# Performance work log

Hardware: AMD Instinct MI355X
Metric: run time of the kernel (lower is better)

Reference implementation:

```python
import jax, jax.numpy as jnp
import numpy as np

N = 50257   # vocab size
D = 128     # embedding_dim
B = 2048    # batch
C = 10      # context window size


def setup_inputs() -> dict:
    key = jax.random.key(0)
    ks = jax.random.split(key, 16)
    s = 0.02
    return {
        "x_batch": jax.random.randint(ks[0], (B,), 0, N),
        "context_words_batch": jax.random.randint(ks[1], (B, C), 0, N),
        "eps": jax.random.normal(ks[2], (B, D), dtype=jnp.float32),
        # learned parameters
        "inf_emb": jax.random.normal(ks[3], (N, D), dtype=jnp.float32) * s,
        "W_aff": jax.random.normal(ks[4], (D, 2 * D), dtype=jnp.float32) * s,
        "b_aff": jnp.zeros((D,), dtype=jnp.float32),
        "W_mu": jax.random.normal(ks[5], (D, D), dtype=jnp.float32) * s,
        "b_mu": jnp.zeros((D,), dtype=jnp.float32),
        "W_sig": jax.random.normal(ks[6], (D, D), dtype=jnp.float32) * s,
        "b_sig": jnp.zeros((D,), dtype=jnp.float32),
        "gen_sigma_emb": jax.random.normal(ks[7], (N, D), dtype=jnp.float32) * s,
        "W_gen": jax.random.normal(ks[8], (N, D), dtype=jnp.float32) * s,
        "b_gen": jnp.zeros((N,), dtype=jnp.float32),
    }


def reference(x_batch, context_words_batch, eps, inf_emb, W_aff, b_aff,
              W_mu, b_mu, W_sig, b_sig, gen_sigma_emb, W_gen, b_gen):
    # ---- inference network (vectorized over batch and context) ----
    center = inf_emb[x_batch]                    # [B, D]
    ctx = inf_emb[context_words_batch]           # [B, C, D]
    center_rep = jnp.broadcast_to(center[:, None, :], ctx.shape)  # [B, C, D]
    cat = jnp.concatenate([center_rep, ctx], axis=-1)             # [B, C, 2D]
    h = jax.nn.relu(jnp.einsum("bce,de->bcd", cat, W_aff) + b_aff)
    h_sum = h.sum(axis=1)                        # [B, D]
    inf_mu = h_sum @ W_mu.T + b_mu               # [B, D]
    inf_sigma = jax.nn.softplus(h_sum @ W_sig.T + b_sig)

    # ---- reparameterized sample ----
    z = inf_mu + eps * inf_sigma                 # [B, D]

    # ---- generative / reconstruction term ----
    logits = z @ W_gen.T + b_gen                 # [B, N] (dominant intermediate)
    logp = jax.nn.log_softmax(logits, axis=-1)
    recon = jnp.take_along_axis(logp, context_words_batch, axis=1).sum(-1)  # [B]

    # ---- KL term (faithful to original, incl. use of generative sigma) ----
    sigma = jax.nn.softplus(gen_sigma_emb[x_batch])  # [B, D]
    kl = (jnp.log(sigma / inf_sigma)
          + (inf_sigma ** 2 + (inf_mu - sigma) ** 2) / (2.0 * sigma ** 2)
          - 0.5).sum(-1)                        # [B]

    return (kl - recon).mean()
```

## Files before the change

kernel.cpp:

```cpp
#include <hip/hip_runtime.h>
#include <float.h>
#include <math.h>

#define NV 50257
#define D 128
#define B 2048
#define C 10

#define NVPAD 50272
#define NTILES (NVPAD / 16)
#define NSTREAM 128
#define NG4 (NVPAD * D / 4)
#define LOG2E 1.44269504088896f
#define SC1 0x7F7F7F7F

typedef __attribute__((ext_vector_type(8))) short short8;
typedef __attribute__((ext_vector_type(8))) int int8v;
typedef __attribute__((ext_vector_type(4))) float float4v;
typedef __attribute__((ext_vector_type(2))) float float2v;

__device__ __forceinline__ float softplus_f(float x) {
    return fmaxf(x, 0.f) + log1pf(expf(-fabsf(x)));
}

__device__ __forceinline__ short f2bf(float f) {
    unsigned u = __float_as_uint(f);
    unsigned r = (u + 0x7FFFu + ((u >> 16) & 1u)) >> 16;
    return (short)r;
}

__global__ __launch_bounds__(256) void k_pre(
    const float* __restrict__ waff, const float* __restrict__ wmu,
    const float* __restrict__ wsig, const float* __restrict__ b_gen,
    short* __restrict__ waff_o, short* __restrict__ wmu_o,
    short* __restrict__ wsig_o, float* __restrict__ bg2, float* __restrict__ out)
{
    const int j = blockIdx.x * 256 + threadIdx.x;
    if (j == 0) out[0] = 0.f;
    if (j < 16384) {
        const float4* src; short4* dst; int jj;
        if (j < 8192)       { src = (const float4*)waff; dst = (short4*)waff_o; jj = j; }
        else if (j < 12288) { src = (const float4*)wmu;  dst = (short4*)wmu_o;  jj = j - 8192; }
        else                { src = (const float4*)wsig; dst = (short4*)wsig_o; jj = j - 12288; }
        const float4 g = src[jj];
        short4 o;
        o.x = f2bf(g.x); o.y = f2bf(g.y); o.z = f2bf(g.z); o.w = f2bf(g.w);
        dst[jj] = o;
    } else {
        const int jj = j - 16384;
        if (jj < NVPAD / 4) {
            const int e0 = jj * 4;
            float4 o;
            o.x = (e0 + 0 < NV) ? b_gen[e0 + 0] * LOG2E : -INFINITY;
            o.y = (e0 + 1 < NV) ? b_gen[e0 + 1] * LOG2E : -INFINITY;
            o.z = (e0 + 2 < NV) ? b_gen[e0 + 2] * LOG2E : -INFINITY;
            o.w = (e0 + 3 < NV) ? b_gen[e0 + 3] * LOG2E : -INFINITY;
            ((float4*)bg2)[jj] = o;
        }
    }
}

#define CONVB 629
__global__ __launch_bounds__(640, 1) void k_main(
    const int* __restrict__ x_batch, const int* __restrict__ ctxw,
    const float* __restrict__ eps, const float* __restrict__ inf_emb,
    const short* __restrict__ waff_bf, const float* __restrict__ b_aff,
    const short* __restrict__ wmu_bf, const float* __restrict__ b_mu,
    const short* __restrict__ wsig_bf, const float* __restrict__ b_sig,
    const float* __restrict__ gen_sig_emb, const float* __restrict__ wg,
    unsigned char* __restrict__ w8,
    float* __restrict__ z_out, unsigned char* __restrict__ z8_out,
    float* __restrict__ kl_out)
{
    const int bid = blockIdx.x;
    const int t = threadIdx.x;

    __shared__ float us[16][132];
    __shared__ float hsp[5][16][132];
    __shared__ float kl_s[8][16];

    if (bid >= 128) {
        const int base = (bid - 128) * (640 * 4) + t;
        #pragma unroll
        for (int k = 0; k < 4; ++k) {
            const int i4 = base + k * 640;
            if (i4 < NG4) {
                const int e0 = i4 * 4;
                int pk = 0;
                if (e0 < NV * D) {
                    const float4 g = ((const float4*)wg)[i4];
                    pk = __builtin_amdgcn_cvt_pk_fp8_f32(g.x, g.y, 0, false);
                    pk = __builtin_amdgcn_cvt_pk_fp8_f32(g.z, g.w, pk, true);
                }
                ((int*)w8)[i4] = pk;
            }
        }
        return;
    }

    const int b0 = bid * 16;
    const int wv = t >> 6;
    const int lane = t & 63;
    const int col16 = lane & 15;
    const int quad = lane >> 4;
    const int brow = b0 + col16;

    const int widx = ctxw[brow * C + wv];
    short8 cx[4];
    #pragma unroll
    for (int ks = 0; ks < 4; ++ks) {
        const float* p = inf_emb + (size_t)widx * D + ks * 32 + quad * 8;
        const float4 g0 = *(const float4*)p;
        const float4 g1 = *(const float4*)(p + 4);
        short8 v;
        v[0] = f2bf(g0.x); v[1] = f2bf(g0.y); v[2] = f2bf(g0.z); v[3] = f2bf(g0.w);
        v[4] = f2bf(g1.x); v[5] = f2bf(g1.y); v[6] = f2bf(g1.z); v[7] = f2bf(g1.w);
        cx[ks] = v;
    }

    if (wv < 8) {
        const int cidx = x_batch[brow];
        short8 ce[4];
        #pragma unroll
        for (int ks = 0; ks < 4; ++ks) {
            const float* p = inf_emb + (size_t)cidx * D + ks * 32 + quad * 8;
            const float4 g0 = *(const float4*)p;
            const float4 g1 = *(const float4*)(p + 4);
            short8 v;
            v[0] = f2bf(g0.x); v[1] = f2bf(g0.y); v[2] = f2bf(g0.z); v[3] = f2bf(g0.w);
            v[4] = f2bf(g1.x); v[5] = f2bf(g1.y); v[6] = f2bf(g1.z); v[7] = f2bf(g1.w);
            ce[ks] = v;
        }
        float4v acc = {0.f, 0.f, 0.f, 0.f};
        #pragma unroll
        for (int ks = 0; ks < 4; ++ks) {
            const short8 bw = *(const short8*)(waff_bf + (wv * 16 + col16) * 256 + ks * 32 + quad * 8);
            acc = __builtin_amdgcn_mfma_f32_16x16x32_bf16(ce[ks], bw, acc, 0, 0, 0);
        }
        #pragma unroll
        for (int r = 0; r < 4; ++r)
            us[quad * 4 + r][wv * 16 + col16] = acc[r];
    }
    __syncthreads();

    float ba[8];
    #pragma unroll
    for (int dt = 0; dt < 8; ++dt) ba[dt] = b_aff[dt * 16 + col16];

    float4v H[8];
    #pragma unroll
    for (int dt = 0; dt < 8; ++dt) {
        float4v a = {0.f, 0.f, 0.f, 0.f};
        #pragma unroll
        for (int ks = 0; ks < 4; ++ks) {
            const short8 bw = *(const short8*)(waff_bf + (dt * 16 + col16) * 256 + 128 + ks * 32 + quad * 8);
            a = __builtin_amdgcn_mfma_f32_16x16x32_bf16(cx[ks], bw, a, 0, 0, 0);
        }
        #pragma unroll
        for (int r = 0; r < 4; ++r) {
            const float u = us[quad * 4 + r][dt * 16 + col16];
            H[dt][r] = fmaxf(u + a[r] + ba[dt], 0.f);
        }
    }

    if (wv < 5) {
        #pragma unroll
        for (int dt = 0; dt < 8; ++dt)
            #pragma unroll
            for (int r = 0; r < 4; ++r)
                hsp[wv][quad * 4 + r][dt * 16 + col16] = H[dt][r];
    }
    __syncthreads();
    if (wv >= 5) {
        #pragma unroll
        for (int dt = 0; dt < 8; ++dt)
            #pragma unroll
            for (int r = 0; r < 4; ++r)
                hsp[wv - 5][quad * 4 + r][dt * 16 + col16] += H[dt][r];
    }
    __syncthreads();

    if (wv < 8) {
        short8 ha[4];
        #pragma unroll
        for (int ks = 0; ks < 4; ++ks) {
            const int off = ks * 32 + quad * 8;
            float4 s0 = {0.f, 0.f, 0.f, 0.f}, s1 = {0.f, 0.f, 0.f, 0.f};
            #pragma unroll
            for (int w = 0; w < 5; ++w) {
                const float4 a0 = *(const float4*)&hsp[w][col16][off];
                const float4 a1 = *(const float4*)&hsp[w][col16][off + 4];
                s0.x += a0.x; s0.y += a0.y; s0.z += a0.z; s0.w += a0.w;
                s1.x += a1.x; s1.y += a1.y; s1.z += a1.z; s1.w += a1.w;
            }
            short8 v;
            v[0] = f2bf(s0.x); v[1] = f2bf(s0.y); v[2] = f2bf(s0.z); v[3] = f2bf(s0.w);
            v[4] = f2bf(s1.x); v[5] = f2bf(s1.y); v[6] = f2bf(s1.z); v[7] = f2bf(s1.w);
            ha[ks] = v;
        }

        int xb2[4];
        #pragma unroll
        for (int r = 0; r < 4; ++r) xb2[r] = x_batch[b0 + quad * 4 + r];

        const int nt = wv;
        float4v mu4 = {0.f, 0.f, 0.f, 0.f};
        float4v sg4 = {0.f, 0.f, 0.f, 0.f};
        #pragma unroll
        for (int ks = 0; ks < 4; ++ks) {
            const short8 bm = *(const short8*)(wmu_bf + (nt * 16 + col16) * 128 + ks * 32 + quad * 8);
            const short8 bs = *(const short8*)(wsig_bf + (nt * 16 + col16) * 128 + ks * 32 + quad * 8);
            mu4 = __builtin_amdgcn_mfma_f32_16x16x32_bf16(ha[ks], bm, mu4, 0, 0, 0);
            sg4 = __builtin_amdgcn_mfma_f32_16x16x32_bf16(ha[ks], bs, sg4, 0, 0, 0);
        }
        const int d = nt * 16 + col16;
        const float bmu = b_mu[d];
        const float bsg = b_sig[d];
        float klp[4];
        #pragma unroll
        for (int r = 0; r < 4; ++r) {
            const int b = b0 + quad * 4 + r;
            const float mu = mu4[r] + bmu;
            const float sg = sg4[r] + bsg;
            const float isig = softplus_f(sg);
            const float e = eps[b * D + d];
            const float zz = fmaf(e, isig, mu);
            z_out[b * D + d] = zz;
            const int pk = __builtin_amdgcn_cvt_pk_fp8_f32(zz * LOG2E, 0.f, 0, false);
            z8_out[b * D + d] = (unsigned char)(pk & 0xFF);
            const float gs = softplus_f(gen_sig_emb[(size_t)xb2[r] * D + d]);
            const float diff = mu - gs;
            klp[r] = logf(gs / isig) + (isig * isig + diff * diff) / (2.f * gs * gs) - 0.5f;
        }
        #pragma unroll
        for (int off = 1; off < 16; off <<= 1)
            #pragma unroll
            for (int r = 0; r < 4; ++r)
                klp[r] += __shfl_xor(klp[r], off, 64);
        if (col16 == 0) {
            #pragma unroll
            for (int r = 0; r < 4; ++r)
                kl_s[wv][quad * 4 + r] = klp[r];
        }
    }
    __syncthreads();
    if (t < 16) {
        float s = 0.f;
        #pragma unroll
        for (int w = 0; w < 8; ++w) s += kl_s[w][t];
        kl_out[b0 + t] = s;
    }
}

#define LOADT8(bf, g, T) { \
    const int v_ = (T) < NTILES; \
    const int tt_ = v_ ? (T) : 0; \
    bf = *(const int8v*)(w8 + (size_t)(tt_ * 16 + col16) * D + quad * 32); \
    g = v_ ? bg2t[tt_ * 16 + col16] : -INFINITY; }

#define COMP8(bf, g) { \
    _Pragma("unroll") \
    for (int rt = 0; rt < 4; ++rt) { \
        float4v c = {g, g, g, g}; \
        c = __builtin_amdgcn_mfma_scale_f32_16x16x128_f8f6f4( \
                afrag[rt], bf, c, 0, 0, 0, SC1, 0, SC1); \
        _Pragma("unroll") \
        for (int r = 0; r < 4; ++r) \
            sums[rt][r] += __builtin_amdgcn_exp2f(c[r]); \
    } }

__global__ __launch_bounds__(256) void k_lse_mfma(
    const unsigned char* __restrict__ z8, const unsigned char* __restrict__ w8,
    const float* __restrict__ bg2t, float* __restrict__ part_s)
{
    const int bid = blockIdx.x;
    const int s = bid & 127;
    const int x = bid >> 7;
    const int t = threadIdx.x;
    const int wv = t >> 6;
    const int lane = t & 63;
    const int col16 = lane & 15;
    const int quad = lane >> 4;
    const int rowbase = x * 256 + wv * 64;

    int8v afrag[4];
    #pragma unroll
    for (int rt = 0; rt < 4; ++rt)
        afrag[rt] = *(const int8v*)(z8 + (size_t)(rowbase + rt * 16 + col16) * D + quad * 32);

    float sums[4][4];
    #pragma unroll
    for (int rt = 0; rt < 4; ++rt)
        #pragma unroll
        for (int r = 0; r < 4; ++r) sums[rt][r] = 0.f;

    int8v bA, bB, bC, bD;
    float gA, gB, gC, gD;
    LOADT8(bA, gA, s);
    LOADT8(bB, gB, s + 128);
    LOADT8(bC, gC, s + 256);
    LOADT8(bD, gD, s + 384);
    #pragma unroll 1
    for (int j = 0; j < 20; j += 4) {
        COMP8(bA, gA); LOADT8(bA, gA, s + (j + 4) * 128);
        COMP8(bB, gB); LOADT8(bB, gB, s + (j + 5) * 128);
        COMP8(bC, gC); LOADT8(bC, gC, s + (j + 6) * 128);
        COMP8(bD, gD); LOADT8(bD, gD, s + (j + 7) * 128);
    }
    COMP8(bA, gA);
    COMP8(bB, gB); COMP8(bC, gC); COMP8(bD, gD);
    LOADT8(bA, gA, s + 24 * 128);
    COMP8(bA, gA);

    #pragma unroll
    for (int off = 1; off < 16; off <<= 1)
        #pragma unroll
        for (int rt = 0; rt < 4; ++rt)
            #pragma unroll
            for (int r = 0; r < 4; ++r)
                sums[rt][r] += __shfl_xor(sums[rt][r], off, 64);

    if (col16 == 0) {
        #pragma unroll
        for (int rt = 0; rt < 4; ++rt)
            #pragma unroll
            for (int r = 0; r < 4; ++r) {
                const int row = rowbase + rt * 16 + quad * 4 + r;
                part_s[row * NSTREAM + s] = sums[rt][r];
            }
    }
}

__global__ __launch_bounds__(256) void k_final(
    const float* __restrict__ z, const unsigned char* __restrict__ w8,
    const float* __restrict__ b_gen, const int* __restrict__ ctxw,
    const float* __restrict__ part_s, const float* __restrict__ kl,
    float* __restrict__ out)
{
    const int t = threadIdx.x;
    const int wv = t >> 6;
    const int lane = t & 63;
    __shared__ float red[4];

    float wsum = 0.f;
    #pragma unroll
    for (int rr = 0; rr < 2; ++rr) {
        const int b = blockIdx.x * 8 + wv * 2 + rr;

        int idxs[C];
        #pragma unroll
        for (int c = 0; c < C; ++c) idxs[c] = ctxw[b * C + c];
        unsigned short uw[C];
        #pragma unroll
        for (int c = 0; c < C; ++c)
            uw[c] = *(const unsigned short*)(w8 + (size_t)idxs[c] * D + lane * 2);
        float sum_bg = 0.f;
        #pragma unroll
        for (int c = 0; c < C; ++c) sum_bg += b_gen[idxs[c]];

        float sv = part_s[b * NSTREAM + lane] + part_s[b * NSTREAM + 64 + lane];
        const float z0 = z[b * D + lane * 2];
        const float z1 = z[b * D + lane * 2 + 1];

        float acc = 0.f;
        #pragma unroll
        for (int c = 0; c < C; ++c) {
            const float2v wf = __builtin_amdgcn_cvt_pk_f32_fp8((int)uw[c], false);
            acc = fmaf(z0, wf[0], acc);
            acc = fmaf(z1, wf[1], acc);
        }
        #pragma unroll
        for (int off = 32; off > 0; off >>= 1) {
            sv  += __shfl_xor(sv, off, 64);
            acc += __shfl_xor(acc, off, 64);
        }
        if (lane == 0) {
            const float lse = logf(sv);
            const float recon = acc + sum_bg - C * lse;
            wsum += kl[b] - recon;
        }
    }
    if (lane == 0) red[wv] = wsum;
    __syncthreads();
    if (t == 0) atomicAdd(out, (red[0] + red[1] + red[2] + red[3]) * (1.f / B));
}

extern "C" void kernel_launch(void* const* d_in, const int* in_sizes, int n_in,
                              void* d_out, int out_size, void* d_ws, size_t ws_size,
                              hipStream_t stream) {
    const int* x_batch = (const int*)d_in[0];
    const int* ctxw    = (const int*)d_in[1];
    const float* eps   = (const float*)d_in[2];
    const float* inf_emb = (const float*)d_in[3];
    const float* W_aff = (const float*)d_in[4];
    const float* b_aff = (const float*)d_in[5];
    const float* W_mu  = (const float*)d_in[6];
    const float* b_mu  = (const float*)d_in[7];
    const float* W_sig = (const float*)d_in[8];
    const float* b_sig = (const float*)d_in[9];
    const float* gen_sig = (const float*)d_in[10];
    const float* W_gen = (const float*)d_in[11];
    const float* b_gen = (const float*)d_in[12];
    float* out = (float*)d_out;

    char* ws = (char*)d_ws;
    float* z      = (float*)ws;   ws += (size_t)B * D * 4;
    float* part_s = (float*)ws;   ws += (size_t)B * NSTREAM * 4;
    float* kl     = (float*)ws;   ws += (size_t)B * 4;
    float* bg2    = (float*)ws;   ws += (size_t)NVPAD * 4;
    unsigned char* z8 = (unsigned char*)ws;  ws += (size_t)B * D;
    unsigned char* w8 = (unsigned char*)ws;  ws += (size_t)NVPAD * D;
    short* waff_bf = (short*)ws;  ws += (size_t)128 * 256 * 2;
    short* wmu_bf  = (short*)ws;  ws += (size_t)128 * 128 * 2;
    short* wsig_bf = (short*)ws;  ws += (size_t)128 * 128 * 2;

    const int pre_items = 16384 + NVPAD / 4;
    hipLaunchKernelGGL(k_pre, dim3((pre_items + 255) / 256), dim3(256), 0, stream,
                       W_aff, W_mu, W_sig, b_gen,
                       waff_bf, wmu_bf, wsig_bf, bg2, out);
    hipLaunchKernelGGL(k_main, dim3(128 + CONVB), dim3(640), 0, stream,
                       x_batch, ctxw, eps, inf_emb, waff_bf, b_aff, wmu_bf, b_mu,
                       wsig_bf, b_sig, gen_sig, W_gen, w8, z, z8, kl);
    hipLaunchKernelGGL(k_lse_mfma, dim3(8 * NSTREAM), dim3(256), 0, stream,
                       z8, w8, bg2, part_s);
    hipLaunchKernelGGL(k_final, dim3(B / 8), dim3(256), 0, stream,
                       z, w8, b_gen, ctxw, part_s, kl, out);
}
```

Baseline: 177.5 us.

## Fuse final reduction into LSE kernel via last-block atomic counter

Merges the final recon/KL reduction kernel into the log-sum-exp MFMA kernel. Each of 128 stream blocks per row group bumps an atomic counter, and the last block to finish processes all 256 rows of that group. Counters are zeroed in the pre kernel. This removes a kernel launch and its gap, but it concentrates the final work in 8 blocks that run serially over 64 rows per wave, which may lengthen the tail.

Result: slower. 365.7 us (+106.0%).

```diff
diff --git a/kernel.cpp b/kernel.cpp
--- a/kernel.cpp
+++ b/kernel.cpp
@@ -33,7 +33,8 @@
     const float* __restrict__ waff, const float* __restrict__ wmu,
     const float* __restrict__ wsig, const float* __restrict__ b_gen,
     short* __restrict__ waff_o, short* __restrict__ wmu_o,
-    short* __restrict__ wsig_o, float* __restrict__ bg2, float* __restrict__ out)
+    short* __restrict__ wsig_o, float* __restrict__ bg2,
+    int* __restrict__ done_cnt, float* __restrict__ out)
 {
     const int j = blockIdx.x * 256 + threadIdx.x;
     if (j == 0) out[0] = 0.f;
@@ -56,6 +57,8 @@
             o.z = (e0 + 2 < NV) ? b_gen[e0 + 2] * LOG2E : -INFINITY;
             o.w = (e0 + 3 < NV) ? b_gen[e0 + 3] * LOG2E : -INFINITY;
             ((float4*)bg2)[jj] = o;
+        } else if (jj < NVPAD / 4 + 8) {
+            done_cnt[jj - NVPAD / 4] = 0;
         }
     }
 }
@@ -269,9 +272,12 @@
             sums[rt][r] += __builtin_amdgcn_exp2f(c[r]); \
     } }
 
-__global__ __launch_bounds__(256) void k_lse_mfma(
+__global__ __launch_bounds__(256) void k_lse_final(
     const unsigned char* __restrict__ z8, const unsigned char* __restrict__ w8,
-    const float* __restrict__ bg2t, float* __restrict__ part_s)
+    const float* __restrict__ bg2t, float* __restrict__ part_s,
+    const float* __restrict__ z, const float* __restrict__ b_gen,
+    const int* __restrict__ ctxw, const float* __restrict__ kl,
+    int* __restrict__ done_cnt, float* __restrict__ out)
 {
     const int bid = blockIdx.x;
     const int s = bid & 127;
@@ -282,6 +288,9 @@
     const int col16 = lane & 15;
     const int quad = lane >> 4;
     const int rowbase = x * 256 + wv * 64;
+
+    __shared__ int is_last;
+    __shared__ float red[4];
 
     int8v afrag[4];
     #pragma unroll
@@ -329,23 +338,20 @@
                 part_s[row * NSTREAM + s] = sums[rt][r];
             }
     }
-}
-
-__global__ __launch_bounds__(256) void k_final(
-    const float* __restrict__ z, const unsigned char* __restrict__ w8,
-    const float* __restrict__ b_gen, const int* __restrict__ ctxw,
-    const float* __restrict__ part_s, const float* __restrict__ kl,
-    float* __restrict__ out)
-{
-    const int t = threadIdx.x;
-    const int wv = t >> 6;
-    const int lane = t & 63;
-    __shared__ float red[4];
+
+    __threadfence();
+    if (t == 0) {
+        const int old = atomicAdd(&done_cnt[x], 1);
+        is_last = (old == 127);
+    }
+    __syncthreads();
+    if (!is_last) return;
+    __threadfence();
 
     float wsum = 0.f;
-    #pragma unroll
-    for (int rr = 0; rr < 2; ++rr) {
-        const int b = blockIdx.x * 8 + wv * 2 + rr;
+    #pragma unroll 2
+    for (int rr = 0; rr < 64; ++rr) {
+        const int b = x * 256 + wv * 64 + rr;
 
         int idxs[C];
         #pragma unroll
@@ -413,16 +419,15 @@
     short* waff_bf = (short*)ws;  ws += (size_t)128 * 256 * 2;
     short* wmu_bf  = (short*)ws;  ws += (size_t)128 * 128 * 2;
     short* wsig_bf = (short*)ws;  ws += (size_t)128 * 128 * 2;
-
-    const int pre_items = 16384 + NVPAD / 4;
+    int* done_cnt  = (int*)ws;    ws += 8 * sizeof(int);
+
+    const int pre_items = 16384 + NVPAD / 4 + 8;
     hipLaunchKernelGGL(k_pre, dim3((pre_items + 255) / 256), dim3(256), 0, stream,
                        W_aff, W_mu, W_sig, b_gen,
-                       waff_bf, wmu_bf, wsig_bf, bg2, out);
+                       waff_bf, wmu_bf, wsig_bf, bg2, done_cnt, out);
     hipLaunchKernelGGL(k_main, dim3(128 + CONVB), dim3(640), 0, stream,
                        x_batch, ctxw, eps, inf_emb, waff_bf, b_aff, wmu_bf, b_mu,
                        wsig_bf, b_sig, gen_sig, W_gen, w8, z, z8, kl);
-    hipLaunchKernelGGL(k_lse_mfma, dim3(8 * NSTREAM), dim3(256), 0, stream,
-                       z8, w8, bg2, part_s);
-    hipLaunchKernelGGL(k_final, dim3(B / 8), dim3(256), 0, stream,
-                       z, w8, b_gen, ctxw, part_s, kl, out);
-}
+    hipLaunchKernelGGL(k_lse_final, dim3(8 * NSTREAM), dim3(256), 0, stream,
+                       z8, w8, bg2, part_s, z, b_gen, ctxw, kl, done_cnt, out);
+}
```

## Give each wave its own 16-row batch tile in the inference stage

Applied to the files above, without the earlier changes.

The inference network in k_main is restructured so each 64-lane wave handles a full 16-row batch tile and loops over all ten context words itself. Register double-buffered embedding loads overlap with the MFMA accumulation, replacing the old split of one context word per wave with cross-wave LDS reduction and several block barriers. Blocks shrink to 256 threads, with 32 inference blocks and 786 W_gen fp8 conversion blocks. This removes the LDS partial-sum traffic and most synchronisation, at the cost of higher register pressure and fewer, longer-running inference waves.

After: 207.7 us. 17.0% more time.

```diff
diff --git a/kernel.cpp b/kernel.cpp
--- a/kernel.cpp
+++ b/kernel.cpp
@@ -14,6 +14,9 @@
 #define LOG2E 1.44269504088896f
 #define SC1 0x7F7F7F7F
 
+#define INFB 32
+#define CONV256B 786
+
 typedef __attribute__((ext_vector_type(8))) short short8;
 typedef __attribute__((ext_vector_type(8))) int int8v;
 typedef __attribute__((ext_vector_type(4))) float float4v;
@@ -28,6 +31,29 @@
     unsigned r = (u + 0x7FFFu + ((u >> 16) & 1u)) >> 16;
     return (short)r;
 }
+
+#define LOADEMB(dst, idx) { \
+    const float* p_ = inf_emb + (size_t)(idx) * D; \
+    _Pragma("unroll") \
+    for (int ks_ = 0; ks_ < 4; ++ks_) { \
+        const float4 g0_ = *(const float4*)(p_ + ks_ * 32 + quad * 8); \
+        const float4 g1_ = *(const float4*)(p_ + ks_ * 32 + quad * 8 + 4); \
+        short8 v_; \
+        v_[0] = f2bf(g0_.x); v_[1] = f2bf(g0_.y); v_[2] = f2bf(g0_.z); v_[3] = f2bf(g0_.w); \
+        v_[4] = f2bf(g1_.x); v_[5] = f2bf(g1_.y); v_[6] = f2bf(g1_.z); v_[7] = f2bf(g1_.w); \
+        dst[ks_] = v_; } }
+
+#define ACCH(cxN) { \
+    _Pragma("unroll") \
+    for (int dt_ = 0; dt_ < 8; ++dt_) { \
+        float4v a_ = {0.f, 0.f, 0.f, 0.f}; \
+        _Pragma("unroll") \
+        for (int ks_ = 0; ks_ < 4; ++ks_) { \
+            const short8 bw_ = *(const short8*)(waff_bf + (dt_ * 16 + col16) * 256 + 128 + ks_ * 32 + quad * 8); \
+            a_ = __builtin_amdgcn_mfma_f32_16x16x32_bf16(cxN[ks_], bw_, a_, 0, 0, 0); } \
+        _Pragma("unroll") \
+        for (int r_ = 0; r_ < 4; ++r_) \
+            H[dt_][r_] += fmaxf(U[dt_][r_] + a_[r_] + ba[dt_], 0.f); } }
 
 __global__ __launch_bounds__(256) void k_pre(
     const float* __restrict__ waff, const float* __restrict__ wmu,
@@ -60,8 +86,7 @@
     }
 }
 
-#define CONVB 629
-__global__ __launch_bounds__(640, 1) void k_main(
+__global__ __launch_bounds__(256, 1) void k_main(
     const int* __restrict__ x_batch, const int* __restrict__ ctxw,
     const float* __restrict__ eps, const float* __restrict__ inf_emb,
     const short* __restrict__ waff_bf, const float* __restrict__ b_aff,
@@ -75,15 +100,13 @@
     const int bid = blockIdx.x;
     const int t = threadIdx.x;
 
-    __shared__ float us[16][132];
-    __shared__ float hsp[5][16][132];
-    __shared__ float kl_s[8][16];
-
-    if (bid >= 128) {
-        const int base = (bid - 128) * (640 * 4) + t;
-        #pragma unroll
-        for (int k = 0; k < 4; ++k) {
-            const int i4 = base + k * 640;
+    __shared__ float h_lds[4][16][132];
+
+    if (bid >= INFB) {
+        const int base = (bid - INFB) * (256 * 8) + t;
+        #pragma unroll
+        for (int k = 0; k < 8; ++k) {
+            const int i4 = base + k * 256;
             if (i4 < NG4) {
                 const int e0 = i4 * 4;
                 int pk = 0;
@@ -98,157 +121,140 @@
         return;
     }
 
-    const int b0 = bid * 16;
     const int wv = t >> 6;
     const int lane = t & 63;
     const int col16 = lane & 15;
     const int quad = lane >> 4;
-    const int brow = b0 + col16;
-
-    const int widx = ctxw[brow * C + wv];
-    short8 cx[4];
+    const int b0 = (bid * 4 + wv) * 16;
+
+    int wi[10];
+    #pragma unroll
+    for (int c = 0; c < 10; ++c) wi[c] = ctxw[(b0 + col16) * C + c];
+    const int cidx = x_batch[b0 + col16];
+
+    short8 ce[4], cx0[4], cx1[4], cx2[4], cx3[4];
+    LOADEMB(ce, cidx);
+    LOADEMB(cx0, wi[0]);
+    LOADEMB(cx1, wi[1]);
+    LOADEMB(cx2, wi[2]);
+    LOADEMB(cx3, wi[3]);
+
+    float ba[8];
+    #pragma unroll
+    for (int dt = 0; dt < 8; ++dt) ba[dt] = b_aff[dt * 16 + col16];
+
+    float4v U[8];
+    #pragma unroll
+    for (int dt = 0; dt < 8; ++dt) {
+        float4v acc = {0.f, 0.f, 0.f, 0.f};
+        #pragma unroll
+        for (int ks = 0; ks < 4; ++ks) {
+            const short8 bw = *(const short8*)(waff_bf + (dt * 16 + col16) * 256 + ks * 32 + quad * 8);
+            acc = __builtin_amdgcn_mfma_f32_16x16x32_bf16(ce[ks], bw, acc, 0, 0, 0);
+        }
+        U[dt] = acc;
+    }
+
+    float4v H[8];
+    #pragma unroll
+    for (int dt = 0; dt < 8; ++dt) H[dt] = (float4v){0.f, 0.f, 0.f, 0.f};
+
+    ACCH(cx0); LOADEMB(cx0, wi[4]);
+    ACCH(cx1); LOADEMB(cx1, wi[5]);
+    ACCH(cx2); LOADEMB(cx2, wi[6]);
+    ACCH(cx3); LOADEMB(cx3, wi[7]);
+    ACCH(cx0); LOADEMB(cx0, wi[8]);
+    ACCH(cx1); LOADEMB(cx1, wi[9]);
+    ACCH(cx2);
+    ACCH(cx3);
+    ACCH(cx0);
+    ACCH(cx1);
+
+    #pragma unroll
+    for (int dt = 0; dt < 8; ++dt)
+        #pragma unroll
+        for (int r = 0; r < 4; ++r)
+            h_lds[wv][quad * 4 + r][dt * 16 + col16] = H[dt][r];
+    __syncthreads();
+
+    short8 ha[4];
     #pragma unroll
     for (int ks = 0; ks < 4; ++ks) {
-        const float* p = inf_emb + (size_t)widx * D + ks * 32 + quad * 8;
-        const float4 g0 = *(const float4*)p;
-        const float4 g1 = *(const float4*)(p + 4);
+        const int off = ks * 32 + quad * 8;
+        const float4 a0 = *(const float4*)&h_lds[wv][col16][off];
+        const float4 a1 = *(const float4*)&h_lds[wv][col16][off + 4];
         short8 v;
-        v[0] = f2bf(g0.x); v[1] = f2bf(g0.y); v[2] = f2bf(g0.z); v[3] = f2bf(g0.w);
-        v[4] = f2bf(g1.x); v[5] = f2bf(g1.y); v[6] = f2bf(g1.z); v[7] = f2bf(g1.w);
-        cx[ks] = v;
-    }
-
-    if (wv < 8) {
-        const int cidx = x_batch[brow];
-        short8 ce[4];
-        #pragma unroll
-        for (int ks = 0; ks < 4; ++ks) {
-            const float* p = inf_emb + (size_t)cidx * D + ks * 32 + quad * 8;
-            const float4 g0 = *(const float4*)p;
-            const float4 g1 = *(const float4*)(p + 4);
-            short8 v;
-            v[0] = f2bf(g0.x); v[1] = f2bf(g0.y); v[2] = f2bf(g0.z); v[3] = f2bf(g0.w);
-            v[4] = f2bf(g1.x); v[5] = f2bf(g1.y); v[6] = f2bf(g1.z); v[7] = f2bf(g1.w);
-            ce[ks] = v;
-        }
-        float4v acc = {0.f, 0.f, 0.f, 0.f};
-        #pragma unroll
-        for (int ks = 0; ks < 4; ++ks) {
-            const short8 bw = *(const short8*)(waff_bf + (wv * 16 + col16) * 256 + ks * 32 + quad * 8);
-            acc = __builtin_amdgcn_mfma_f32_16x16x32_bf16(ce[ks], bw, acc, 0, 0, 0);
-        }
+        v[0] = f2bf(a0.x); v[1] = f2bf(a0.y); v[2] = f2bf(a0.z); v[3] = f2bf(a0.w);
+        v[4] = f2bf(a1.x); v[5] = f2bf(a1.y); v[6] = f2bf(a1.z); v[7] = f2bf(a1.w);
+        ha[ks] = v;
+    }
+
+    int xb2[4];
+    #pragma unroll
+    for (int r = 0; r < 4; ++r) xb2[r] = x_batch[b0 + quad * 4 + r];
+
+    float klp[4] = {0.f, 0.f, 0.f, 0.f};
+
+    #pragma unroll
+    for (int half = 0; half < 2; ++half) {
+        float gsr[4][4], epr[4][4];
+        #pragma unroll
+        for (int n = 0; n < 4; ++n) {
+            const int d = (half * 4 + n) * 16 + col16;
+            #pragma unroll
+            for (int r = 0; r < 4; ++r) {
+                gsr[n][r] = gen_sig_emb[(size_t)xb2[r] * D + d];
+                epr[n][r] = eps[(b0 + quad * 4 + r) * D + d];
+            }
+        }
+
+        float4v mu[4], sg[4];
+        #pragma unroll
+        for (int n = 0; n < 4; ++n) {
+            const int nt = half * 4 + n;
+            float4v m_ = {0.f, 0.f, 0.f, 0.f};
+            float4v s_ = {0.f, 0.f, 0.f, 0.f};
+            #pragma unroll
+            for (int ks = 0; ks < 4; ++ks) {
+                const short8 bm = *(const short8*)(wmu_bf  + (nt * 16 + col16) * 128 + ks * 32 + quad * 8);
+                const short8 bs = *(const short8*)(wsig_bf + (nt * 16 + col16) * 128 + ks * 32 + quad * 8);
+                m_ = __builtin_amdgcn_mfma_f32_16x16x32_bf16(ha[ks], bm, m_, 0, 0, 0);
+                s_ = __builtin_amdgcn_mfma_f32_16x16x32_bf16(ha[ks], bs, s_, 0, 0, 0);
+            }
+            mu[n] = m_; sg[n] = s_;
+        }
+
+        #pragma unroll
+        for (int n = 0; n < 4; ++n) {
+            const int d = (half * 4 + n) * 16 + col16;
+            const float bmu = b_mu[d];
+            const float bsg = b_sig[d];
+            #pragma unroll
+            for (int r = 0; r < 4; ++r) {
+                const int b = b0 + quad * 4 + r;
+                const float m = mu[n][r] + bmu;
+                const float s = sg[n][r] + bsg;
+                const float isig = softplus_f(s);
+                const float zz = fmaf(epr[n][r], isig, m);
+                z_out[b * D + d] = zz;
+                const int pk = __builtin_amdgcn_cvt_pk_fp8_f32(zz * LOG2E, 0.f, 0, false);
+                z8_out[b * D + d] = (unsigned char)(pk & 0xFF);
+                const float gs = softplus_f(gsr[n][r]);
+                const float diff = m - gs;
+                klp[r] += logf(gs / isig) + (isig * isig + diff * diff) / (2.f * gs * gs) - 0.5f;
+            }
+        }
+    }
+
+    #pragma unroll
+    for (int off = 1; off < 16; off <<= 1)
         #pragma unroll
         for (int r = 0; r < 4; ++r)
-            us[quad * 4 + r][wv * 16 + col16] = acc[r];
-    }
-    __syncthreads();
-
-    float ba[8];
-    #pragma unroll
-    for (int dt = 0; dt < 8; ++dt) ba[dt] = b_aff[dt * 16 + col16];
-
-    float4v H[8];
-    #pragma unroll
-    for (int dt = 0; dt < 8; ++dt) {
-        float4v a = {0.f, 0.f, 0.f, 0.f};
-        #pragma unroll
-        for (int ks = 0; ks < 4; ++ks) {
-            const short8 bw = *(const short8*)(waff_bf + (dt * 16 + col16) * 256 + 128 + ks * 32 + quad * 8);
-            a = __builtin_amdgcn_mfma_f32_16x16x32_bf16(cx[ks], bw, a, 0, 0, 0);
-        }
-        #pragma unroll
-        for (int r = 0; r < 4; ++r) {
-            const float u = us[quad * 4 + r][dt * 16 + col16];
-            H[dt][r] = fmaxf(u + a[r] + ba[dt], 0.f);
-        }
-    }
-
-    if (wv < 5) {
-        #pragma unroll
-        for (int dt = 0; dt < 8; ++dt)
-            #pragma unroll
-            for (int r = 0; r < 4; ++r)
-                hsp[wv][quad * 4 + r][dt * 16 + col16] = H[dt][r];
-    }
-    __syncthreads();
-    if (wv >= 5) {
-        #pragma unroll
-        for (int dt = 0; dt < 8; ++dt)
-            #pragma unroll
-            for (int r = 0; r < 4; ++r)
-                hsp[wv - 5][quad * 4 + r][dt * 16 + col16] += H[dt][r];
-    }
-    __syncthreads();
-
-    if (wv < 8) {
-        short8 ha[4];
-        #pragma unroll
-        for (int ks = 0; ks < 4; ++ks) {
-            const int off = ks * 32 + quad * 8;
-            float4 s0 = {0.f, 0.f, 0.f, 0.f}, s1 = {0.f, 0.f, 0.f, 0.f};
-            #pragma unroll
-            for (int w = 0; w < 5; ++w) {
-                const float4 a0 = *(const float4*)&hsp[w][col16][off];
-                const float4 a1 = *(const float4*)&hsp[w][col16][off + 4];
-                s0.x += a0.x; s0.y += a0.y; s0.z += a0.z; s0.w += a0.w;
-                s1.x += a1.x; s1.y += a1.y; s1.z += a1.z; s1.w += a1.w;
-            }
-            short8 v;
-            v[0] = f2bf(s0.x); v[1] = f2bf(s0.y); v[2] = f2bf(s0.z); v[3] = f2bf(s0.w);
-            v[4] = f2bf(s1.x); v[5] = f2bf(s1.y); v[6] = f2bf(s1.z); v[7] = f2bf(s1.w);
-            ha[ks] = v;
-        }
-
-        int xb2[4];
-        #pragma unroll
-        for (int r = 0; r < 4; ++r) xb2[r] = x_batch[b0 + quad * 4 + r];
-
-        const int nt = wv;
-        float4v mu4 = {0.f, 0.f, 0.f, 0.f};
-        float4v sg4 = {0.f, 0.f, 0.f, 0.f};
-        #pragma unroll
-        for (int ks = 0; ks < 4; ++ks) {
-            const short8 bm = *(const short8*)(wmu_bf + (nt * 16 + col16) * 128 + ks * 32 + quad * 8);
-            const short8 bs = *(const short8*)(wsig_bf + (nt * 16 + col16) * 128 + ks * 32 + quad * 8);
-            mu4 = __builtin_amdgcn_mfma_f32_16x16x32_bf16(ha[ks], bm, mu4, 0, 0, 0);
-            sg4 = __builtin_amdgcn_mfma_f32_16x16x32_bf16(ha[ks], bs, sg4, 0, 0, 0);
-        }
-        const int d = nt * 16 + col16;
-        const float bmu = b_mu[d];
-        const float bsg = b_sig[d];
-        float klp[4];
-        #pragma unroll
-        for (int r = 0; r < 4; ++r) {
-            const int b = b0 + quad * 4 + r;
-            const float mu = mu4[r] + bmu;
-            const float sg = sg4[r] + bsg;
-            const float isig = softplus_f(sg);
-            const float e = eps[b * D + d];
-            const float zz = fmaf(e, isig, mu);
-            z_out[b * D + d] = zz;
-            const int pk = __builtin_amdgcn_cvt_pk_fp8_f32(zz * LOG2E, 0.f, 0, false);
-            z8_out[b * D + d] = (unsigned char)(pk & 0xFF);
-            const float gs = softplus_f(gen_sig_emb[(size_t)xb2[r] * D + d]);
-            const float diff = mu - gs;
-            klp[r] = logf(gs / isig) + (isig * isig + diff * diff) / (2.f * gs * gs) - 0.5f;
-        }
-        #pragma unroll
-        for (int off = 1; off < 16; off <<= 1)
-            #pragma unroll
-            for (int r = 0; r < 4; ++r)
-                klp[r] += __shfl_xor(klp[r], off, 64);
-        if (col16 == 0) {
-            #pragma unroll
-            for (int r = 0; r < 4; ++r)
-                kl_s[wv][quad * 4 + r] = klp[r];
-        }
-    }
-    __syncthreads();
-    if (t < 16) {
-        float s = 0.f;
-        #pragma unroll
-        for (int w = 0; w < 8; ++w) s += kl_s[w][t];
-        kl_out[b0 + t] = s;
+            klp[r] += __shfl_xor(klp[r], off, 64);
+    if (col16 == 0) {
+        #pragma unroll
+        for (int r = 0; r < 4; ++r)
+            kl_out[b0 + quad * 4 + r] = klp[r];
     }
 }
 
@@ -418,7 +424,7 @@
     hipLaunchKernelGGL(k_pre, dim3((pre_items + 255) / 256), dim3(256), 0, stream,
                        W_aff, W_mu, W_sig, b_gen,
                        waff_bf, wmu_bf, wsig_bf, bg2, out);
-    hipLaunchKernelGGL(k_main, dim3(128 + CONVB), dim3(640), 0, stream,
+    hipLaunchKernelGGL(k_main, dim3(INFB + CONV256B), dim3(256), 0, stream,
                        x_batch, ctxw, eps, inf_emb, waff_bf, b_aff, wmu_bf, b_mu,
                        wsig_bf, b_sig, gen_sig, W_gen, w8, z, z8, kl);
     hipLaunchKernelGGL(k_lse_mfma, dim3(8 * NSTREAM), dim3(256), 0, stream,
```
